# Kernel optimization log

Hardware: AMD Instinct MI355X
Metric: run time of the kernel (lower is better)

Reference implementation:

```python
import jax, jax.numpy as jnp
import numpy as np

N = 50000
E = 800000
IN_DIM, HID_DIM, OUT_DIM = 128, 64, 32


def _gcn_layer(x, src, dst, norm, W, b, n):
    # GCNConv: h = D^{-1/2}(A+I)D^{-1/2} (x W) + b
    h = x @ W  # [n, d_out]
    agg = jax.ops.segment_sum(h[src] * norm[:, None], dst, num_segments=n)
    return agg + b


def _backbone(x, edge_index, W1, b1, W2, b2):
    n = x.shape[0]
    loop = jnp.arange(n)
    src = jnp.concatenate([edge_index[0], loop])  # add self-loops
    dst = jnp.concatenate([edge_index[1], loop])
    deg = jax.ops.segment_sum(jnp.ones(src.shape[0], x.dtype), dst, num_segments=n)
    dinv = jax.lax.rsqrt(deg)  # deg >= 1 thanks to self-loops
    norm = dinv[src] * dinv[dst]  # symmetric normalization per edge
    h = jax.nn.relu(_gcn_layer(x, src, dst, norm, W1, b1, n))
    return _gcn_layer(h, src, dst, norm, W2, b2, n)


def _zscore_cols(h):
    # torch: (h - h.mean(0)) / h.std(0), std is unbiased (ddof=1)
    mean = h.mean(0)
    std = jnp.sqrt(jnp.sum((h - mean) ** 2, axis=0) / (h.shape[0] - 1))
    return (h - mean) / std


def setup_inputs() -> dict:
    key = jax.random.key(0)
    k1, k2, k3, k4, k5, k6 = jax.random.split(key, 6)
    x1 = jax.random.normal(k1, (N, IN_DIM), dtype=jnp.float32)
    x2 = jax.random.normal(k2, (N, IN_DIM), dtype=jnp.float32)
    edge_index1 = jax.random.randint(k3, (2, E), 0, N, dtype=jnp.int64 if jax.config.jax_enable_x64 else jnp.int32)
    edge_index2 = jax.random.randint(k4, (2, E), 0, N, dtype=jnp.int64 if jax.config.jax_enable_x64 else jnp.int32)
    W1 = jax.random.normal(k5, (IN_DIM, HID_DIM), dtype=jnp.float32) * (1.0 / np.sqrt(IN_DIM))
    W2 = jax.random.normal(k6, (HID_DIM, OUT_DIM), dtype=jnp.float32) * (1.0 / np.sqrt(HID_DIM))
    b1 = jnp.zeros((HID_DIM,), jnp.float32)
    b2 = jnp.zeros((OUT_DIM,), jnp.float32)
    return {"x1": x1, "edge_index1": edge_index1, "x2": x2, "edge_index2": edge_index2,
            "W1": W1, "b1": b1, "W2": W2, "b2": b2}


def reference(x1, edge_index1, x2, edge_index2, W1, b1, W2, b2):
    h1 = _backbone(x1, edge_index1, W1, b1, W2, b2)
    h2 = _backbone(x2, edge_index2, W1, b1, W2, b2)
    z1 = _zscore_cols(h1)
    z2 = _zscore_cols(h2)
    return (z1, z2)
```

## Files before the change

kernel.cpp:

```cpp
#include <hip/hip_runtime.h>
#include <hip/hip_fp16.h>
#include <math.h>

#define IN_DIM 128
#define HID 64
#define OUTD 32
#define BSH 8
#define BSZ 256
#define EPB 4096
#define XPAD 136
#define NCOPY 16

typedef __attribute__((ext_vector_type(8))) _Float16 f16x8;
typedef __attribute__((ext_vector_type(4))) float f32x4;

struct GB {
    const int* src; const int* dst;
    int* bh;
    int* btot;
    unsigned int* pairs;
    int* rowptr; int* csr_src;
    float* dinv;
    double* st;
    float* og;
    _Float16* o16;
    const float* x;
    _Float16* hs;
    __half* h2;
};

__global__ void __launch_bounds__(256) k_p1(GB g0, GB g1, const float* __restrict__ W,
                                            int e, int n, int nb, int nbh, int nmm) {
    __shared__ char smem[2 * 64 * XPAD * 2];
    int tid = threadIdx.x;
    int bx = blockIdx.x;
    if (bx < 2 * nbh) {
        const GB& g = (bx >= nbh) ? g1 : g0;
        int blk = (bx >= nbh) ? bx - nbh : bx;
        int* hist = (int*)smem;
        for (int i = tid; i < nb; i += 256) hist[i] = 0;
        __syncthreads();
        int base = blk * EPB;
#pragma unroll
        for (int k = 0; k < EPB / 256; ++k) {
            int idx = base + k * 256 + tid;
            if (idx < e) atomicAdd(&hist[g.dst[idx] >> BSH], 1);
        }
        __syncthreads();
        int* row = g.bh + (size_t)blk * nb;
        for (int i = tid; i < nb; i += 256) row[i] = hist[i];
    } else {
        int mx = bx - 2 * nbh;
        const GB& g = (mx >= nmm) ? g1 : g0;
        int blk = (mx >= nmm) ? mx - nmm : mx;
        _Float16 (*xs)[XPAD] = (_Float16(*)[XPAD])smem;
        _Float16 (*wt)[XPAD] = (_Float16(*)[XPAD])(smem + 64 * XPAD * 2);
        int node0 = blk * 64;
        {
            const float4* W4 = (const float4*)W;
#pragma unroll
            for (int j = 0; j < 8; ++j) {
                int idx4 = tid + 256 * j;
                float4 w = W4[idx4];
                int k = idx4 >> 4;
                int d = (idx4 & 15) * 4;
                wt[d][k]     = (_Float16)w.x;
                wt[d + 1][k] = (_Float16)w.y;
                wt[d + 2][k] = (_Float16)w.z;
                wt[d + 3][k] = (_Float16)w.w;
            }
        }
        {
            const float4* X4 = (const float4*)g.x;
#pragma unroll
            for (int j = 0; j < 8; ++j) {
                int i = tid + 256 * j;
                int row = i >> 5, c4 = i & 31;
                int gn = node0 + row;
                float4 v = (gn < n) ? X4[(size_t)gn * 32 + c4] : make_float4(0.f, 0.f, 0.f, 0.f);
                _Float16* p = &xs[row][c4 * 4];
                p[0] = (_Float16)v.x; p[1] = (_Float16)v.y;
                p[2] = (_Float16)v.z; p[3] = (_Float16)v.w;
            }
        }
        __syncthreads();
        int wv = tid >> 6, lane = tid & 63;
        int r16 = lane & 15, khi = lane >> 4;
        int wnode0 = wv * 16;
        f32x4 acc[4] = {};
#pragma unroll
        for (int kk = 0; kk < 4; ++kk) {
            f16x8 a = *(const f16x8*)&xs[wnode0 + r16][kk * 32 + khi * 8];
#pragma unroll
            for (int nt = 0; nt < 4; ++nt) {
                f16x8 b = *(const f16x8*)&wt[nt * 16 + r16][kk * 32 + khi * 8];
                acc[nt] = __builtin_amdgcn_mfma_f32_16x16x32_f16(a, b, acc[nt], 0, 0, 0);
            }
        }
#pragma unroll
        for (int r = 0; r < 4; ++r) {
            int node = node0 + wnode0 + khi * 4 + r;
            if (node < n) {
#pragma unroll
                for (int nt = 0; nt < 4; ++nt)
                    g.hs[(size_t)node * HID + nt * 16 + r16] = (_Float16)acc[nt][r];
            }
        }
    }
}

__global__ void k_colscan(GB g0, GB g1, int nb, int nbh) {
    const GB& g = blockIdx.y ? g1 : g0;
    __shared__ int ls[256];
    int tid = threadIdx.x;
    int b = blockIdx.x;
    int v = (tid < nbh) ? g.bh[(size_t)tid * nb + b] : 0;
    ls[tid] = v;
    __syncthreads();
    for (int off = 1; off < 256; off <<= 1) {
        int u = (tid >= off) ? ls[tid - off] : 0;
        __syncthreads();
        ls[tid] += u;
        __syncthreads();
    }
    if (tid < nbh) g.bh[(size_t)tid * nb + b] = ls[tid] - v;
    if (tid == 255) g.btot[b] = ls[255];
    if (b < 4) {
        int i = b * 256 + tid;
        g.st[i] = 0.0;
    }
}

__global__ void __launch_bounds__(256) k_part2(GB g0, GB g1, int e, int nb, int nbh) {
    int bx = blockIdx.x;
    const GB& g = ((bx & 7) >= 4) ? g1 : g0;
    int blk = (bx >> 3) * 4 + (bx & 3);
    if (blk >= nbh) return;
    __shared__ int sc[256];
    __shared__ int lcur[512];
    int tid = threadIdx.x;
    int v = (tid < nb) ? g.btot[tid] : 0;
    sc[tid] = v;
    __syncthreads();
    for (int off = 1; off < 256; off <<= 1) {
        int u = (tid >= off) ? sc[tid - off] : 0;
        __syncthreads();
        sc[tid] += u;
        __syncthreads();
    }
    int excl = sc[tid] - v;
    __syncthreads();
    sc[tid] = excl;
    __syncthreads();
    const int* row = g.bh + (size_t)blk * nb;
    for (int i = tid; i < nb; i += 256) lcur[i] = sc[i] + row[i];
    __syncthreads();
    int base = blk * EPB;
#pragma unroll
    for (int k = 0; k < EPB / 256; ++k) {
        int idx = base + k * 256 + tid;
        if (idx < e) {
            int s = g.src[idx], d = g.dst[idx];
            int pos = atomicAdd(&lcur[d >> BSH], 1);
            g.pairs[pos] = (unsigned int)s | ((unsigned int)(d & (BSZ - 1)) << 24);
        }
    }
}

__global__ void __launch_bounds__(256) k_local_csr(GB g0, GB g1, int n, int e, int nb) {
    int bx = blockIdx.x;
    const GB& g = ((bx & 7) >= 4) ? g1 : g0;
    int b = (bx >> 3) * 4 + (bx & 3);
    if (b >= nb) return;
    __shared__ int sc[256], ldeg[BSZ], lrow[BSZ];
    __shared__ float ldv[BSZ];
    int tid = threadIdx.x;
    int v = (tid < nb) ? g.btot[tid] : 0;
    sc[tid] = v;
    __syncthreads();
    for (int off = 1; off < 256; off <<= 1) {
        int u = (tid >= off) ? sc[tid - off] : 0;
        __syncthreads();
        sc[tid] += u;
        __syncthreads();
    }
    int excl = sc[tid] - v;
    __syncthreads();
    sc[tid] = excl;
    __syncthreads();
    int node0 = b << BSH;
    int lo = sc[b], hi = lo + g.btot[b];
    ldeg[tid] = 0;
    __syncthreads();
    for (int j = lo + tid; j < hi; j += 256)
        atomicAdd(&ldeg[g.pairs[j] >> 24], 1);
    __syncthreads();
    int d = ldeg[tid];
    lrow[tid] = d;
    __syncthreads();
    for (int off = 1; off < BSZ; off <<= 1) {
        int u = (tid >= off) ? lrow[tid - off] : 0;
        __syncthreads();
        lrow[tid] += u;
        __syncthreads();
    }
    int node = node0 + tid;
    if (node < n) {
        g.rowptr[node] = lo + lrow[tid] - d;
        float dvv = rsqrtf((float)(d + 1));
        g.dinv[node] = dvv;
        ldv[tid] = dvv;
    } else {
        ldv[tid] = 0.0f;
    }
    lrow[tid] = lo + lrow[tid] - d;
    __syncthreads();
    for (int j = lo + tid; j < hi; j += 256) {
        unsigned int w = g.pairs[j];
        int pos = atomicAdd(&lrow[w >> 24], 1);
        g.csr_src[pos] = (int)(w & 0xFFFFFFu);
    }
    if (b == 0 && tid == 0) g.rowptr[n] = e;
    __half2* Hv = (__half2*)g.hs;
    for (int i = tid; i < BSZ * (HID / 2); i += 256) {
        int row = i >> 5;
        int nd = node0 + row;
        if (nd < n) {
            float scv = ldv[row];
            size_t idx = (size_t)nd * (HID / 2) + (i & 31);
            float2 vv = __half22float2(Hv[idx]);
            Hv[idx] = __floats2half2_rn(vv.x * scv, vv.y * scv);
        }
    }
}

__global__ void __launch_bounds__(256) k_gather_fuse(GB g0, GB g1, const float* __restrict__ b1,
                                                     const float* __restrict__ W2, int n, int nblkg) {
    int bx = blockIdx.x;
    const GB& g = ((bx & 7) >= 4) ? g1 : g0;
    int blk = (bx >> 3) * 4 + (bx & 3);
    if (blk >= nblkg) return;
    __shared__ float sh[32][HID + 1];
    __shared__ float w2s[HID][OUTD];
    __shared__ float bs[HID];
    int tid = threadIdx.x;
    for (int i = tid; i < HID * OUTD; i += 256) w2s[i >> 5][i & 31] = W2[i];
    if (tid < HID) bs[tid] = b1[tid];
    int l8 = tid & 7, gi = tid >> 3;
    int node = blk * 32 + gi;
    float a[8] = {};
    if (node < n) {
        const f16x8* H = (const f16x8*)g.hs;
        f16x8 v = H[(size_t)node * 8 + l8];
#pragma unroll
        for (int k = 0; k < 8; ++k) a[k] = (float)v[k];
        int lo = g.rowptr[node], hi = g.rowptr[node + 1];
        int j = lo;
        for (; j + 8 <= hi; j += 8) {
            int s0 = g.csr_src[j],     s1 = g.csr_src[j + 1];
            int s2 = g.csr_src[j + 2], s3 = g.csr_src[j + 3];
            int s4 = g.csr_src[j + 4], s5 = g.csr_src[j + 5];
            int s6 = g.csr_src[j + 6], s7 = g.csr_src[j + 7];
            f16x8 v0 = H[(size_t)s0 * 8 + l8];
            f16x8 v1 = H[(size_t)s1 * 8 + l8];
            f16x8 v2 = H[(size_t)s2 * 8 + l8];
            f16x8 v3 = H[(size_t)s3 * 8 + l8];
            f16x8 v4 = H[(size_t)s4 * 8 + l8];
            f16x8 v5 = H[(size_t)s5 * 8 + l8];
            f16x8 v6 = H[(size_t)s6 * 8 + l8];
            f16x8 v7 = H[(size_t)s7 * 8 + l8];
            f16x8 s01 = v0 + v1, s23 = v2 + v3, s45 = v4 + v5, s67 = v6 + v7;
            f16x8 s = (s01 + s23) + (s45 + s67);
#pragma unroll
            for (int k = 0; k < 8; ++k) a[k] += (float)s[k];
        }
        if (j + 4 <= hi) {
            int s0 = g.csr_src[j],     s1 = g.csr_src[j + 1];
            int s2 = g.csr_src[j + 2], s3 = g.csr_src[j + 3];
            f16x8 v0 = H[(size_t)s0 * 8 + l8];
            f16x8 v1 = H[(size_t)s1 * 8 + l8];
            f16x8 v2 = H[(size_t)s2 * 8 + l8];
            f16x8 v3 = H[(size_t)s3 * 8 + l8];
            f16x8 s = (v0 + v1) + (v2 + v3);
#pragma unroll
            for (int k = 0; k < 8; ++k) a[k] += (float)s[k];
            j += 4;
        }
        for (; j < hi; ++j) {
            f16x8 v0 = H[(size_t)g.csr_src[j] * 8 + l8];
#pragma unroll
            for (int k = 0; k < 8; ++k) a[k] += (float)v0[k];
        }
    }
    __syncthreads();
    if (node < n) {
        float dv = g.dinv[node];
#pragma unroll
        for (int k = 0; k < 8; ++k)
            a[k] = fmaxf(fmaf(a[k], dv, bs[l8 * 8 + k]), 0.0f);
    }
#pragma unroll
    for (int k = 0; k < 8; ++k) sh[gi][l8 * 8 + k] = a[k];
    __syncthreads();
    int n2 = tid >> 3, fo = (tid & 7) * 4;
    int node2 = blk * 32 + n2;
    if (node2 < n) {
        float a0 = 0.f, a1 = 0.f, a2 = 0.f, a3 = 0.f;
#pragma unroll
        for (int k = 0; k < HID; ++k) {
            float s = sh[n2][k];
            a0 = fmaf(s, w2s[k][fo], a0);
            a1 = fmaf(s, w2s[k][fo + 1], a1);
            a2 = fmaf(s, w2s[k][fo + 2], a2);
            a3 = fmaf(s, w2s[k][fo + 3], a3);
        }
        float dv2 = g.dinv[node2];
        __half2* H2 = (__half2*)g.h2;
        H2[(size_t)node2 * (OUTD / 2) + (fo >> 1)]     = __floats2half2_rn(a0 * dv2, a1 * dv2);
        H2[(size_t)node2 * (OUTD / 2) + (fo >> 1) + 1] = __floats2half2_rn(a2 * dv2, a3 * dv2);
    }
}

__global__ void __launch_bounds__(256) k_gather2s(GB g0, GB g1, int n, int nblkg) {
    int bx = blockIdx.x;
    const GB& g = ((bx & 7) >= 4) ? g1 : g0;
    int blk = (bx >> 3) * 4 + (bx & 3);
    if (blk >= nblkg) return;
    __shared__ float sx[64][33], sq[64][33];
    int tid = threadIdx.x;
    int l4 = tid & 3, gi = tid >> 2;
    int node = blk * 64 + gi;
    float a[8] = {};
    if (node < n) {
        const f16x8* H = (const f16x8*)g.h2;
        f16x8 v = H[(size_t)node * 4 + l4];
#pragma unroll
        for (int k = 0; k < 8; ++k) a[k] = (float)v[k];
        int lo = g.rowptr[node], hi = g.rowptr[node + 1];
        int j = lo;
        for (; j + 8 <= hi; j += 8) {
            int s0 = g.csr_src[j],     s1 = g.csr_src[j + 1];
            int s2 = g.csr_src[j + 2], s3 = g.csr_src[j + 3];
            int s4 = g.csr_src[j + 4], s5 = g.csr_src[j + 5];
            int s6 = g.csr_src[j + 6], s7 = g.csr_src[j + 7];
            f16x8 v0 = H[(size_t)s0 * 4 + l4];
            f16x8 v1 = H[(size_t)s1 * 4 + l4];
            f16x8 v2 = H[(size_t)s2 * 4 + l4];
            f16x8 v3 = H[(size_t)s3 * 4 + l4];
            f16x8 v4 = H[(size_t)s4 * 4 + l4];
            f16x8 v5 = H[(size_t)s5 * 4 + l4];
            f16x8 v6 = H[(size_t)s6 * 4 + l4];
            f16x8 v7 = H[(size_t)s7 * 4 + l4];
            f16x8 s01 = v0 + v1, s23 = v2 + v3, s45 = v4 + v5, s67 = v6 + v7;
            f16x8 s = (s01 + s23) + (s45 + s67);
#pragma unroll
            for (int k = 0; k < 8; ++k) a[k] += (float)s[k];
        }
        if (j + 4 <= hi) {
            int s0 = g.csr_src[j],     s1 = g.csr_src[j + 1];
            int s2 = g.csr_src[j + 2], s3 = g.csr_src[j + 3];
            f16x8 v0 = H[(size_t)s0 * 4 + l4];
            f16x8 v1 = H[(size_t)s1 * 4 + l4];
            f16x8 v2 = H[(size_t)s2 * 4 + l4];
            f16x8 v3 = H[(size_t)s3 * 4 + l4];
            f16x8 s = (v0 + v1) + (v2 + v3);
#pragma unroll
            for (int k = 0; k < 8; ++k) a[k] += (float)s[k];
            j += 4;
        }
        for (; j < hi; ++j) {
            f16x8 v0 = H[(size_t)g.csr_src[j] * 4 + l4];
#pragma unroll
            for (int k = 0; k < 8; ++k) a[k] += (float)v0[k];
        }
        float dv = g.dinv[node];
#pragma unroll
        for (int k = 0; k < 8; ++k) a[k] *= dv;
        f16x8 o;
#pragma unroll
        for (int k = 0; k < 8; ++k) o[k] = (_Float16)a[k];
        ((f16x8*)g.o16)[(size_t)node * 4 + l4] = o;
    }
#pragma unroll
    for (int k = 0; k < 8; ++k) {
        sx[gi][l4 * 8 + k] = a[k];
        sq[gi][l4 * 8 + k] = a[k] * a[k];
    }
    __syncthreads();
    if (tid < 64) {
        int c = tid & 31;
        bool isq = tid >= 32;
        float s = 0.0f;
        for (int r = 0; r < 64; ++r) s += isq ? sq[r][c] : sx[r][c];
        atomicAdd(&g.st[(blk & (NCOPY - 1)) * 64 + c + (isq ? 32 : 0)], (double)s);
    }
}

__global__ void k_transform(GB g0, GB g1, int n) {
    const GB& g = blockIdx.y ? g1 : g0;
    __shared__ float fm[32], fr[32];
    int tid = threadIdx.x;
    if (tid < 32) {
        double sum = 0.0, sqs = 0.0;
#pragma unroll
        for (int k = 0; k < NCOPY; ++k) {
            sum += g.st[k * 64 + tid];
            sqs += g.st[k * 64 + tid + 32];
        }
        double mean = sum / (double)n;
        double var = (sqs - sum * sum / (double)n) / (double)(n - 1);
        fm[tid] = (float)mean;
        fr[tid] = (float)(1.0 / sqrt(var));
    }
    __syncthreads();
    int t4 = (blockIdx.x * 256 + tid) * 4;
    if (t4 < n * OUTD) {
        const __half2* O = (const __half2*)g.o16;
        float2 u0 = __half22float2(O[t4 / 2]);
        float2 u1 = __half22float2(O[t4 / 2 + 1]);
        int c = t4 & 31;
        float4 r;
        r.x = (u0.x - fm[c])     * fr[c];
        r.y = (u0.y - fm[c + 1]) * fr[c + 1];
        r.z = (u1.x - fm[c + 2]) * fr[c + 2];
        r.w = (u1.y - fm[c + 3]) * fr[c + 3];
        *(float4*)&g.og[t4] = r;
    }
}


extern "C" void kernel_launch(void* const* d_in, const int* in_sizes, int n_in,
                              void* d_out, int out_size, void* d_ws, size_t ws_size,
                              hipStream_t stream) {
    const float* x1 = (const float*)d_in[0];
    const int*   ei1 = (const int*)d_in[1];
    const float* x2 = (const float*)d_in[2];
    const int*   ei2 = (const int*)d_in[3];
    const float* W1 = (const float*)d_in[4];
    const float* b1 = (const float*)d_in[5];
    const float* W2 = (const float*)d_in[6];
    const float* b2 = (const float*)d_in[7];
    (void)b2;
    (void)n_in; (void)out_size; (void)ws_size;

    int n = in_sizes[0] / IN_DIM;
    int e = in_sizes[1] / 2;
    float* out = (float*)d_out;
    int nb  = (n + BSZ - 1) >> BSH;
    int nbh = (e + EPB - 1) / EPB;
    int nmm = (n + 63) / 64;

    char* ws = (char*)d_ws;
    size_t off = 0;
    auto alloc = [&](size_t bytes) {
        void* p = ws + off;
        off = (off + bytes + 255) & ~(size_t)255;
        return p;
    };
    int*    bh_base   = (int*)alloc((size_t)2 * nbh * nb * 4);
    int*    btot_base = (int*)alloc((size_t)2 * nb * 4);
    double* st_base   = (double*)alloc((size_t)2 * NCOPY * 64 * 8);
    _Float16* o16_base = (_Float16*)alloc((size_t)2 * n * OUTD * 2);

    GB G[2];
    for (int g = 0; g < 2; ++g) {
        const int* ei = g ? ei2 : ei1;
        G[g].src  = ei;
        G[g].dst  = ei + e;
        G[g].x    = g ? x2 : x1;
        G[g].bh   = bh_base + (size_t)g * nbh * nb;
        G[g].btot = btot_base + (size_t)g * nb;
        G[g].st   = st_base + (size_t)g * NCOPY * 64;
        G[g].o16  = o16_base + (size_t)g * n * OUTD;
        G[g].rowptr  = (int*)alloc(((size_t)n + 1) * 4);
        G[g].csr_src = (int*)alloc((size_t)e * 4);
        G[g].dinv    = (float*)alloc((size_t)n * 4);
        G[g].og      = out + (size_t)g * n * OUTD;
        G[g].hs      = (_Float16*)alloc((size_t)n * HID * 2);
    }
    size_t pairs_bytes = (size_t)2 * e * 4;
    size_t h2_bytes    = (size_t)2 * n * OUTD * 2;
    char* uni = (char*)alloc(pairs_bytes > h2_bytes ? pairs_bytes : h2_bytes);
    G[0].pairs = (unsigned int*)uni;
    G[1].pairs = G[0].pairs + e;
    G[0].h2 = (__half*)uni;
    G[1].h2 = G[0].h2 + (size_t)n * OUTD;

    k_p1<<<dim3(2 * nbh + 2 * nmm), 256, 0, stream>>>(G[0], G[1], W1, e, n, nb, nbh, nmm);
    k_colscan<<<dim3(nb, 2), 256, 0, stream>>>(G[0], G[1], nb, nbh);
    int slotsP = ((nbh + 3) / 4) * 8;
    k_part2<<<dim3(slotsP), 256, 0, stream>>>(G[0], G[1], e, nb, nbh);
    int slotsC = ((nb + 3) / 4) * 8;
    k_local_csr<<<dim3(slotsC), BSZ, 0, stream>>>(G[0], G[1], n, e, nb);

    int nblkg1 = (n + 31) / 32;
    int slots1 = ((nblkg1 + 3) / 4) * 8;
    k_gather_fuse<<<dim3(slots1), 256, 0, stream>>>(G[0], G[1], b1, W2, n, nblkg1);
    int nblkg2 = (n + 63) / 64;
    int slots2 = ((nblkg2 + 3) / 4) * 8;
    k_gather2s<<<dim3(slots2), 256, 0, stream>>>(G[0], G[1], n, nblkg2);

    k_transform<<<dim3((n * OUTD / 4 + 255) / 256, 2), 256, 0, stream>>>(G[0], G[1], n);
}
```

Measured before the change: 121.5 us.

## Move X·W1 matmul from histogram kernel into scatter-partition kernel, pretranspose W1

The dense X·W1 MFMA matmul blocks now share a launch with the edge scatter-partition pass instead of the histogram pass. The histogram kernel gets one extra block that converts W1 to a transposed fp16 copy in workspace, so matmul blocks load it with vector copies rather than converting it themselves. The aim is to keep the tiny histogram launch short and overlap the heavier matmul with the atomic-bound scatter. Scatter blocks now run in a kernel with a larger shared-memory footprint, which may lower their occupancy.

```diff
diff --git a/kernel.cpp b/kernel.cpp
--- a/kernel.cpp
+++ b/kernel.cpp
@@ -29,45 +29,106 @@
     __half* h2;
 };
 
-__global__ void __launch_bounds__(256) k_p1(GB g0, GB g1, const float* __restrict__ W,
-                                            int e, int n, int nb, int nbh, int nmm) {
+__global__ void __launch_bounds__(256) k_hist(GB g0, GB g1, const float* __restrict__ W,
+                                              _Float16* __restrict__ wt16, int e, int nb, int nbh) {
+    int tid = threadIdx.x;
+    int bx = blockIdx.x;
+    if (bx == 2 * nbh) {
+        for (int i = tid; i < HID * IN_DIM; i += 256) {
+            int d = i >> 7, k = i & 127;
+            wt16[i] = (_Float16)W[k * HID + d];
+        }
+        return;
+    }
+    const GB& g = (bx >= nbh) ? g1 : g0;
+    int blk = (bx >= nbh) ? bx - nbh : bx;
+    __shared__ int hist[512];
+    for (int i = tid; i < nb; i += 256) hist[i] = 0;
+    __syncthreads();
+    int base = blk * EPB;
+#pragma unroll
+    for (int k = 0; k < EPB / 256; ++k) {
+        int idx = base + k * 256 + tid;
+        if (idx < e) atomicAdd(&hist[g.dst[idx] >> BSH], 1);
+    }
+    __syncthreads();
+    int* row = g.bh + (size_t)blk * nb;
+    for (int i = tid; i < nb; i += 256) row[i] = hist[i];
+}
+
+__global__ void k_colscan(GB g0, GB g1, int nb, int nbh) {
+    const GB& g = blockIdx.y ? g1 : g0;
+    __shared__ int ls[256];
+    int tid = threadIdx.x;
+    int b = blockIdx.x;
+    int v = (tid < nbh) ? g.bh[(size_t)tid * nb + b] : 0;
+    ls[tid] = v;
+    __syncthreads();
+    for (int off = 1; off < 256; off <<= 1) {
+        int u = (tid >= off) ? ls[tid - off] : 0;
+        __syncthreads();
+        ls[tid] += u;
+        __syncthreads();
+    }
+    if (tid < nbh) g.bh[(size_t)tid * nb + b] = ls[tid] - v;
+    if (tid == 255) g.btot[b] = ls[255];
+    if (b < 4) {
+        int i = b * 256 + tid;
+        g.st[i] = 0.0;
+    }
+}
+
+__global__ void __launch_bounds__(256) k_p2mm(GB g0, GB g1, const _Float16* __restrict__ wt16,
+                                              int e, int n, int nb, int nbh, int slotsP, int nmm) {
     __shared__ char smem[2 * 64 * XPAD * 2];
     int tid = threadIdx.x;
     int bx = blockIdx.x;
-    if (bx < 2 * nbh) {
-        const GB& g = (bx >= nbh) ? g1 : g0;
-        int blk = (bx >= nbh) ? bx - nbh : bx;
-        int* hist = (int*)smem;
-        for (int i = tid; i < nb; i += 256) hist[i] = 0;
+    if (bx < slotsP) {
+        const GB& g = ((bx & 7) >= 4) ? g1 : g0;
+        int blk = (bx >> 3) * 4 + (bx & 3);
+        if (blk >= nbh) return;
+        int* sc = (int*)smem;
+        int* lcur = (int*)(smem + 1024);
+        int v = (tid < nb) ? g.btot[tid] : 0;
+        sc[tid] = v;
+        __syncthreads();
+        for (int off = 1; off < 256; off <<= 1) {
+            int u = (tid >= off) ? sc[tid - off] : 0;
+            __syncthreads();
+            sc[tid] += u;
+            __syncthreads();
+        }
+        int excl = sc[tid] - v;
+        __syncthreads();
+        sc[tid] = excl;
+        __syncthreads();
+        const int* row = g.bh + (size_t)blk * nb;
+        for (int i = tid; i < nb; i += 256) lcur[i] = sc[i] + row[i];
         __syncthreads();
         int base = blk * EPB;
 #pragma unroll
         for (int k = 0; k < EPB / 256; ++k) {
             int idx = base + k * 256 + tid;
-            if (idx < e) atomicAdd(&hist[g.dst[idx] >> BSH], 1);
-        }
-        __syncthreads();
-        int* row = g.bh + (size_t)blk * nb;
-        for (int i = tid; i < nb; i += 256) row[i] = hist[i];
+            if (idx < e) {
+                int s = g.src[idx], d = g.dst[idx];
+                int pos = atomicAdd(&lcur[d >> BSH], 1);
+                g.pairs[pos] = (unsigned int)s | ((unsigned int)(d & (BSZ - 1)) << 24);
+            }
+        }
     } else {
-        int mx = bx - 2 * nbh;
+        int mx = bx - slotsP;
         const GB& g = (mx >= nmm) ? g1 : g0;
         int blk = (mx >= nmm) ? mx - nmm : mx;
         _Float16 (*xs)[XPAD] = (_Float16(*)[XPAD])smem;
         _Float16 (*wt)[XPAD] = (_Float16(*)[XPAD])(smem + 64 * XPAD * 2);
         int node0 = blk * 64;
         {
-            const float4* W4 = (const float4*)W;
-#pragma unroll
-            for (int j = 0; j < 8; ++j) {
-                int idx4 = tid + 256 * j;
-                float4 w = W4[idx4];
-                int k = idx4 >> 4;
-                int d = (idx4 & 15) * 4;
-                wt[d][k]     = (_Float16)w.x;
-                wt[d + 1][k] = (_Float16)w.y;
-                wt[d + 2][k] = (_Float16)w.z;
-                wt[d + 3][k] = (_Float16)w.w;
+            const f16x8* Wg = (const f16x8*)wt16;
+#pragma unroll
+            for (int j = 0; j < 4; ++j) {
+                int i = tid + 256 * j;
+                int d = i >> 4, koff = (i & 15) * 8;
+                *(f16x8*)&wt[d][koff] = Wg[i];
             }
         }
         {
@@ -105,64 +166,6 @@
                 for (int nt = 0; nt < 4; ++nt)
                     g.hs[(size_t)node * HID + nt * 16 + r16] = (_Float16)acc[nt][r];
             }
-        }
-    }
-}
-
-__global__ void k_colscan(GB g0, GB g1, int nb, int nbh) {
-    const GB& g = blockIdx.y ? g1 : g0;
-    __shared__ int ls[256];
-    int tid = threadIdx.x;
-    int b = blockIdx.x;
-    int v = (tid < nbh) ? g.bh[(size_t)tid * nb + b] : 0;
-    ls[tid] = v;
-    __syncthreads();
-    for (int off = 1; off < 256; off <<= 1) {
-        int u = (tid >= off) ? ls[tid - off] : 0;
-        __syncthreads();
-        ls[tid] += u;
-        __syncthreads();
-    }
-    if (tid < nbh) g.bh[(size_t)tid * nb + b] = ls[tid] - v;
-    if (tid == 255) g.btot[b] = ls[255];
-    if (b < 4) {
-        int i = b * 256 + tid;
-        g.st[i] = 0.0;
-    }
-}
-
-__global__ void __launch_bounds__(256) k_part2(GB g0, GB g1, int e, int nb, int nbh) {
-    int bx = blockIdx.x;
-    const GB& g = ((bx & 7) >= 4) ? g1 : g0;
-    int blk = (bx >> 3) * 4 + (bx & 3);
-    if (blk >= nbh) return;
-    __shared__ int sc[256];
-    __shared__ int lcur[512];
-    int tid = threadIdx.x;
-    int v = (tid < nb) ? g.btot[tid] : 0;
-    sc[tid] = v;
-    __syncthreads();
-    for (int off = 1; off < 256; off <<= 1) {
-        int u = (tid >= off) ? sc[tid - off] : 0;
-        __syncthreads();
-        sc[tid] += u;
-        __syncthreads();
-    }
-    int excl = sc[tid] - v;
-    __syncthreads();
-    sc[tid] = excl;
-    __syncthreads();
-    const int* row = g.bh + (size_t)blk * nb;
-    for (int i = tid; i < nb; i += 256) lcur[i] = sc[i] + row[i];
-    __syncthreads();
-    int base = blk * EPB;
-#pragma unroll
-    for (int k = 0; k < EPB / 256; ++k) {
-        int idx = base + k * 256 + tid;
-        if (idx < e) {
-            int s = g.src[idx], d = g.dst[idx];
-            int pos = atomicAdd(&lcur[d >> BSH], 1);
-            g.pairs[pos] = (unsigned int)s | ((unsigned int)(d & (BSZ - 1)) << 24);
         }
     }
 }
@@ -461,6 +464,7 @@
     int*    btot_base = (int*)alloc((size_t)2 * nb * 4);
     double* st_base   = (double*)alloc((size_t)2 * NCOPY * 64 * 8);
     _Float16* o16_base = (_Float16*)alloc((size_t)2 * n * OUTD * 2);
+    _Float16* wt16     = (_Float16*)alloc((size_t)HID * IN_DIM * 2);
 
     GB G[2];
     for (int g = 0; g < 2; ++g) {
@@ -486,10 +490,10 @@
     G[0].h2 = (__half*)uni;
     G[1].h2 = G[0].h2 + (size_t)n * OUTD;
 
-    k_p1<<<dim3(2 * nbh + 2 * nmm), 256, 0, stream>>>(G[0], G[1], W1, e, n, nb, nbh, nmm);
+    k_hist<<<dim3(2 * nbh + 1), 256, 0, stream>>>(G[0], G[1], W1, wt16, e, nb, nbh);
     k_colscan<<<dim3(nb, 2), 256, 0, stream>>>(G[0], G[1], nb, nbh);
     int slotsP = ((nbh + 3) / 4) * 8;
-    k_part2<<<dim3(slotsP), 256, 0, stream>>>(G[0], G[1], e, nb, nbh);
+    k_p2mm<<<dim3(slotsP + 2 * nmm), 256, 0, stream>>>(G[0], G[1], wt16, e, n, nb, nbh, slotsP, nmm);
     int slotsC = ((nb + 3) / 4) * 8;
     k_local_csr<<<dim3(slotsC), BSZ, 0, stream>>>(G[0], G[1], n, e, nb);
 
```

Result: faster. 119.1 us, median of 2 (-2.0%).
